# Kernel optimization log

Measured on AMD Instinct MI355X. Metric: run time of the kernel, lower is better.

The kernel has to match this reference:

```python
import jax, jax.numpy as jnp
import numpy as np

STRIDE = 2
IN_CH = 64
F_SCALE = 2
EMBED = 64  # int(in_ch * ss_exp_factor)


def _pixel_unshuffle(x, f):
    # out[b, (fi*f+fj)*c + cc, h, w] = x[b, cc, h*f+fi, w*f+fj]
    b, c, H, W = x.shape
    x = x.reshape(b, c, H // f, f, W // f, f)
    x = x.transpose(0, 3, 5, 1, 2, 4)  # b, fi, fj, c, h, w
    return x.reshape(b, f * f * c, H // f, W // f)


def _pixel_shuffle(x, f):
    b, fc, h, w = x.shape
    c = fc // (f * f)
    x = x.reshape(b, f, f, c, h, w)
    x = x.transpose(0, 3, 4, 1, 5, 2)  # b, c, h, fi, w, fj
    return x.reshape(b, c, h * f, w * f)


def _conv(x, w, b, dilation):
    out = jax.lax.conv_general_dilated(
        x, w, window_strides=(1, 1),
        padding=[(dilation, dilation), (dilation, dilation)],
        rhs_dilation=(dilation, dilation),
        dimension_numbers=('NCHW', 'OIHW', 'NCHW'))
    return out + b[None, :, None, None]


def _conv1x1(x, w, b):
    out = jax.lax.conv_general_dilated(
        x, w, window_strides=(1, 1), padding=[(0, 0), (0, 0)],
        dimension_numbers=('NCHW', 'OIHW', 'NCHW'))
    return out + b[None, :, None, None]


def _attention(x, wqk, f):
    b, c, H, W = x.shape
    # layer_norm over (c,h,w), no affine
    mu = jnp.mean(x, axis=(1, 2, 3), keepdims=True)
    var = jnp.var(x, axis=(1, 2, 3), keepdims=True)
    xx = (x - mu) / jnp.sqrt(var + 1e-5)
    ph, pw = (f - H % f) % f, (f - W % f) % f
    if ph or pw:
        xx = jnp.pad(xx, ((0, 0), (0, 0), (0, ph), (0, pw)))
        xv = jnp.pad(x, ((0, 0), (0, 0), (0, ph), (0, pw)))
    else:
        xv = x
    sh, sw = (H + ph) // f, (W + pw) // f
    B = b * f * f
    xu = _pixel_unshuffle(xx, f).reshape(B, c, sh, sw)
    vu = _pixel_unshuffle(xv, f).reshape(B, c, sh, sw)
    n = sh * sw
    qk = xu.transpose(0, 2, 3, 1).reshape(B, n, c)  # (B, n, c)
    v = vu.transpose(0, 2, 3, 1).reshape(B, n, c)
    q = qk @ wqk  # (B, n, e)
    q = q / jnp.maximum(jnp.linalg.norm(q, axis=-1, keepdims=True), 1e-12)
    attn = jnp.einsum('bne,bme->bnm', q, q) / jnp.sqrt(jnp.float32(wqk.shape[1]))
    attn = jax.nn.softmax(attn, axis=-1)
    out = jnp.einsum('bnm,bmc->bnc', attn, v)  # (B, n, c)
    out = out.reshape(B, sh, sw, c).transpose(0, 3, 1, 2)
    out = out.reshape(b, f * f * c, sh, sw)
    out = _pixel_shuffle(out, f)
    return out[:, :, :H, :W]


def setup_inputs() -> dict:
    key = jax.random.key(0)
    ks = jax.random.split(key, 8)
    c = IN_CH
    s3 = 1.0 / np.sqrt(c * 9)
    s1 = 1.0 / np.sqrt(c)
    return {
        'x': jax.random.normal(ks[0], (8, c, 128, 128), dtype=jnp.float32),
        'wqk': jax.random.normal(ks[1], (c, EMBED), dtype=jnp.float32) * np.sqrt(6.0 / (c + EMBED)),
        'conv1_w': jax.random.normal(ks[2], (c, c, 3, 3), dtype=jnp.float32) * s3,
        'conv1_b': jnp.zeros((c,), dtype=jnp.float32),
        'conv2_w': jax.random.normal(ks[3], (c, c, 3, 3), dtype=jnp.float32) * s3,
        'conv2_b': jnp.zeros((c,), dtype=jnp.float32),
        'conv3_w': jax.random.normal(ks[4], (c, c, 1, 1), dtype=jnp.float32) * s1,
        'conv3_b': jnp.zeros((c,), dtype=jnp.float32),
    }


def reference(x, wqk, conv1_w, conv1_b, conv2_w, conv2_b, conv3_w, conv3_b):
    f = F_SCALE * STRIDE
    a = x + _attention(x, wqk, f)
    y = jax.nn.relu(_conv(a, conv1_w, conv1_b, STRIDE))
    y = jax.nn.relu(_conv(y, conv2_w, conv2_b, STRIDE))
    y = _conv1x1(y, conv3_w, conv3_b)
    return x + y
```

## Files before the change

kernel.cpp:

```cpp
#include <hip/hip_runtime.h>

typedef unsigned short u16;
typedef unsigned int   u32;

typedef __attribute__((ext_vector_type(8))) short s16x8;
typedef __attribute__((ext_vector_type(4))) float f32x4;

__device__ __forceinline__ float bf2f(u16 u){
  union { u32 i; float f; } v; v.i = ((u32)u) << 16; return v.f;
}
__device__ __forceinline__ u16 f2bf(float f){
  union { float f; u32 i; } v; v.f = f;
  u32 x = v.i;
  return (u16)((x + 0x7fffu + ((x >> 16) & 1u)) >> 16);
}


__global__ __launch_bounds__(256) void k_lnstats(const float* __restrict__ x, float* __restrict__ stats){
  const int bb    = blockIdx.x >> 7;
  const int chunk = blockIdx.x & 127;
  const float4* p = (const float4*)(x + bb*1048576 + chunk*8192);
  float s = 0.f, ss = 0.f;
  #pragma unroll
  for (int i=0;i<8;++i){
    float4 v = p[threadIdx.x + (i<<8)];
    s  += v.x + v.y + v.z + v.w;
    ss += v.x*v.x + v.y*v.y + v.z*v.z + v.w*v.w;
  }
  #pragma unroll
  for (int off=32; off; off>>=1){ s += __shfl_down(s, off); ss += __shfl_down(ss, off); }
  __shared__ float rs[4], rss[4];
  const int lane = threadIdx.x & 63, wv = threadIdx.x >> 6;
  if (lane == 0){ rs[wv] = s; rss[wv] = ss; }
  __syncthreads();
  if (threadIdx.x == 0){
    atomicAdd(&stats[bb*2+0], rs[0]+rs[1]+rs[2]+rs[3]);
    atomicAdd(&stats[bb*2+1], rss[0]+rss[1]+rss[2]+rss[3]);
  }
}

__global__ __launch_bounds__(256) void k_wt(const float* __restrict__ w, u16* __restrict__ wt){
  int e = blockIdx.x*256 + threadIdx.x;
  int tap = e >> 12, co = (e >> 6) & 63, ci = e & 63;
  wt[e] = f2bf(w[(co*64 + ci)*9 + tap]);
}

__global__ __launch_bounds__(256) void k_qv(const float* __restrict__ x, const float* __restrict__ wqk,
                                            const float* __restrict__ stats,
                                            u16* __restrict__ qb, u16* __restrict__ vb){
  const int Bb = blockIdx.x >> 4;
  const int mt = blockIdx.x & 15;
  const int b = Bb >> 4, fi = (Bb >> 2) & 3, fj = Bb & 3;
  const float inv_n = 1.f/1048576.f;
  const float mu   = stats[2*b] * inv_n;
  const float var  = stats[2*b+1]*inv_n - mu*mu;
  const float rstd = rsqrtf(var + 1e-5f);

  __shared__ float xt[64][68];
  __shared__ float wk[64][68];
  __shared__ float red[64][17];
  const int t = threadIdx.x;
  const int m0 = mt << 6;

  #pragma unroll
  for (int i=0;i<16;++i){ int e = t+(i<<8); wk[e>>6][e&63] = wqk[e]; }
  #pragma unroll
  for (int i=0;i<16;++i){
    int e = t+(i<<8); int cc = e>>6, ml = e&63;
    int m = m0 + ml;
    int hh = ((m>>5)<<2)+fi, ww = ((m&31)<<2)+fj;
    xt[ml][cc] = (x[(((b<<6)+cc)<<14)+(hh<<7)+ww] - mu)*rstd;
  }
  __syncthreads();

  const int ty = t>>4, tx = t&15;
  float acc[4][4] = {};
  for (int cc=0; cc<64; ++cc){
    float a0=xt[(ty<<2)+0][cc], a1=xt[(ty<<2)+1][cc], a2=xt[(ty<<2)+2][cc], a3=xt[(ty<<2)+3][cc];
    float b0=wk[cc][(tx<<2)+0], b1=wk[cc][(tx<<2)+1], b2=wk[cc][(tx<<2)+2], b3=wk[cc][(tx<<2)+3];
    acc[0][0]+=a0*b0; acc[0][1]+=a0*b1; acc[0][2]+=a0*b2; acc[0][3]+=a0*b3;
    acc[1][0]+=a1*b0; acc[1][1]+=a1*b1; acc[1][2]+=a1*b2; acc[1][3]+=a1*b3;
    acc[2][0]+=a2*b0; acc[2][1]+=a2*b1; acc[2][2]+=a2*b2; acc[2][3]+=a2*b3;
    acc[3][0]+=a3*b0; acc[3][1]+=a3*b1; acc[3][2]+=a3*b2; acc[3][3]+=a3*b3;
  }
  #pragma unroll
  for (int i=0;i<4;++i){
    float pn = acc[i][0]*acc[i][0]+acc[i][1]*acc[i][1]+acc[i][2]*acc[i][2]+acc[i][3]*acc[i][3];
    red[(ty<<2)+i][tx] = pn;
  }
  __syncthreads();
  float inv[4];
  #pragma unroll
  for (int i=0;i<4;++i){
    float s = 0.f;
    #pragma unroll
    for (int k=0;k<16;++k) s += red[(ty<<2)+i][k];
    inv[i] = 1.f / fmaxf(sqrtf(s), 1e-12f);
  }
  #pragma unroll
  for (int i=0;i<4;++i)
    #pragma unroll
    for (int j=0;j<4;++j)
      xt[(ty<<2)+i][(tx<<2)+j] = acc[i][j]*inv[i];
  __syncthreads();
  #pragma unroll
  for (int i=0;i<16;++i){
    int e = t+(i<<8); int ml = e>>6, ee = e&63;
    qb[((Bb<<10)+m0+ml)*64 + ee] = f2bf(xt[ml][ee]);
  }
  #pragma unroll
  for (int i=0;i<16;++i){
    int e = t+(i<<8); int cc = e>>6, ml = e&63;
    int m = m0 + ml;
    int hh = ((m>>5)<<2)+fi, ww = ((m&31)<<2)+fj;
    wk[ml][cc] = x[(((b<<6)+cc)<<14)+(hh<<7)+ww];
  }
  __syncthreads();
  #pragma unroll
  for (int i=0;i<16;++i){
    int e = t+(i<<8); int cc = e>>6, ml = e&63;
    vb[(Bb<<16) + (cc<<10) + m0 + ml] = f2bf(wk[ml][cc]);
  }
}

__global__ __launch_bounds__(256) void k_attn(const u16* __restrict__ qb, const u16* __restrict__ vb,
                                              const float* __restrict__ x, u16* __restrict__ apad){
  const int bid = blockIdx.x;
  const int b   = bid & 7;
  const int rem = bid >> 3;
  const int qtp = rem >> 4;
  const int sub = rem & 15;
  const int Bb  = (b<<4) + sub;
  const int fi = (sub>>2)&3, fj = sub&3;
  const int qt0 = qtp << 1;
  __shared__ __align__(16) char lds[24576];
  const int KS = 0, VS = 8192, PS = 16384;

  const int t = threadIdx.x;
  const int w = t >> 6, lane = t & 63;
  const int lrow = lane & 15, lk = lane >> 4;

  const u16* qB = qb + (Bb<<16);
  const u16* vB = vb + (Bb<<16);

  s16x8 qf[2][2];
  #pragma unroll
  for (int t2=0; t2<2; ++t2){
    const u16* qrp = qB + (((qt0+t2)<<6) + (w<<4) + lrow)*64;
    qf[t2][0] = *(const s16x8*)(qrp + (lk<<3));
    qf[t2][1] = *(const s16x8*)(qrp + 32 + (lk<<3));
  }

  f32x4 o_acc[2][4] = {};
  float lp[2][4] = {};

  for (int kt=0; kt<16; ++kt){
    __syncthreads();
    #pragma unroll
    for (int c = t; c < 512; c += 256){
      int row = c >> 3, slot = c & 7;
      uint4 kv = *(const uint4*)(qB + ((kt<<6)+row)*64 + (slot<<3));
      *(uint4*)(lds + KS + row*128 + (((slot ^ (row&7)))<<4)) = kv;
      uint4 vv = *(const uint4*)(vB + (row<<10) + (kt<<6) + (slot<<3));
      *(uint4*)(lds + VS + row*128 + (((slot ^ (row&7)))<<4)) = vv;
    }
    __syncthreads();

    #pragma unroll
    for (int t2=0; t2<2; ++t2){
      f32x4 s_acc[4] = {};
      #pragma unroll
      for (int nt=0; nt<4; ++nt){
        int key = (nt<<4) + lrow;
        const char* kb = lds + KS + key*128;
        s16x8 kf0 = *(const s16x8*)(kb + ((lk       ^ (key&7))<<4));
        s16x8 kf1 = *(const s16x8*)(kb + (((4+lk)   ^ (key&7))<<4));
        s_acc[nt] = __builtin_amdgcn_mfma_f32_16x16x32_bf16(qf[t2][0], kf0, s_acc[nt], 0,0,0);
        s_acc[nt] = __builtin_amdgcn_mfma_f32_16x16x32_bf16(qf[t2][1], kf1, s_acc[nt], 0,0,0);
      }
      #pragma unroll
      for (int nt=0; nt<4; ++nt)
        #pragma unroll
        for (int r=0; r<4; ++r){
          float p = __expf(s_acc[nt][r]*0.125f);
          lp[t2][r] += p;
          int prow = (w<<4) + (lk<<2) + r;
          int key  = (nt<<4) + lrow;
          *(u16*)(lds + PS + prow*128 + ((key<<1) ^ ((prow&7)<<4))) = f2bf(p);
        }
      {
        int prow = (w<<4) + lrow;
        const char* pb = lds + PS + prow*128;
        s16x8 pf0 = *(const s16x8*)(pb + ((lk     ^ (prow&7))<<4));
        s16x8 pf1 = *(const s16x8*)(pb + (((4+lk) ^ (prow&7))<<4));
        #pragma unroll
        for (int nt=0; nt<4; ++nt){
          int ch = (nt<<4) + lrow;
          const char* vbp = lds + VS + ch*128;
          s16x8 vf0 = *(const s16x8*)(vbp + ((lk     ^ (ch&7))<<4));
          s16x8 vf1 = *(const s16x8*)(vbp + (((4+lk) ^ (ch&7))<<4));
          o_acc[t2][nt] = __builtin_amdgcn_mfma_f32_16x16x32_bf16(pf0, vf0, o_acc[t2][nt], 0,0,0);
          o_acc[t2][nt] = __builtin_amdgcn_mfma_f32_16x16x32_bf16(pf1, vf1, o_acc[t2][nt], 0,0,0);
        }
      }
    }
  }

  #pragma unroll
  for (int t2=0; t2<2; ++t2)
    #pragma unroll
    for (int r=0;r<4;++r){
      float s = lp[t2][r];
      s += __shfl_xor(s, 1); s += __shfl_xor(s, 2);
      s += __shfl_xor(s, 4); s += __shfl_xor(s, 8);
      lp[t2][r] = 1.f / s;
    }

  float* os = (float*)lds;
  #pragma unroll
  for (int t2=0; t2<2; ++t2){
    __syncthreads();
    #pragma unroll
    for (int nt=0; nt<4; ++nt)
      #pragma unroll
      for (int r=0; r<4; ++r)
        os[((w<<4)+(lk<<2)+r)*68 + (nt<<4)+lrow] = o_acc[t2][nt][r]*lp[t2][r];
    __syncthreads();
    const int m0 = (qt0+t2) << 6;
    #pragma unroll
    for (int i=0;i<16;++i){
      int e = t+(i<<8);
      int cc = e>>6, ml = e&63;
      int m = m0 + ml;
      int hh = ((m>>5)<<2)+fi, ww = ((m&31)<<2)+fj;
      os[ml*68 + cc] += x[(((b<<6)+cc)<<14) + (hh<<7) + ww];
    }
    __syncthreads();
    #pragma unroll
    for (int i=0;i<16;++i){
      int e = t+(i<<8);
      int ml = e>>6, cc = e&63;
      int m = m0 + ml;
      int hh = ((m>>5)<<2)+fi, ww = ((m&31)<<2)+fj;
      apad[((b*132 + hh+2)*132 + ww+2)*64 + cc] = f2bf(os[ml*68 + cc]);
    }
  }
}

__global__ __launch_bounds__(256) void k_conv3m(const u16* __restrict__ in, const u16* __restrict__ wt,
                                                const float* __restrict__ bias, u16* __restrict__ outp){
  const int bid = blockIdx.x;
  const int b   = bid & 7;
  const int r   = bid >> 3;
  const int h   = r & 127;
  const int seg = r >> 7;
  const int t = threadIdx.x;
  const int wv = t >> 6, lane = t & 63;
  const int lrow = lane & 15, lk = lane >> 4;
  const int co0 = wv << 4;
  const int w0 = seg << 6;

  s16x8 A[9][2];
  #pragma unroll
  for (int tap=0; tap<9; ++tap)
    #pragma unroll
    for (int hf=0; hf<2; ++hf)
      A[tap][hf] = *(const s16x8*)(wt + (((tap<<6) + co0 + lrow)<<6) + (hf<<5) + (lk<<3));

  float4 b4 = *(const float4*)&bias[co0 + (lk<<2)];
  f32x4 binit = {b4.x, b4.y, b4.z, b4.w};
  f32x4 acc[4] = {binit, binit, binit, binit};

  const int base_b = b * (132*132);
  #pragma unroll
  for (int dh=0; dh<3; ++dh){
    const u16* rowp = in + ((base_b + (h + (dh<<1))*132)<<6);
    #pragma unroll
    for (int dw=0; dw<3; ++dw){
      #pragma unroll
      for (int hf=0; hf<2; ++hf){
        #pragma unroll
        for (int pt=0; pt<4; ++pt){
          int wp = w0 + (pt<<4) + lrow + (dw<<1);
          s16x8 B = *(const s16x8*)(rowp + (wp<<6) + (hf<<5) + (lk<<3));
          acc[pt] = __builtin_amdgcn_mfma_f32_16x16x32_bf16(A[dh*3+dw][hf], B, acc[pt], 0,0,0);
        }
      }
    }
  }

  #pragma unroll
  for (int pt=0; pt<4; ++pt){
    int wp = w0 + (pt<<4) + lrow + 2;
    u16* op = outp + ((base_b + (h+2)*132 + wp)<<6) + co0 + (lk<<2);
    ushort4 o4;
    o4.x = f2bf(fmaxf(acc[pt][0], 0.f));
    o4.y = f2bf(fmaxf(acc[pt][1], 0.f));
    o4.z = f2bf(fmaxf(acc[pt][2], 0.f));
    o4.w = f2bf(fmaxf(acc[pt][3], 0.f));
    *(ushort4*)op = o4;
  }
}

__global__ __launch_bounds__(256) void k_conv1x1(const u16* __restrict__ y2, const float* __restrict__ w3,
                                                 const float* __restrict__ b3, const float* __restrict__ x,
                                                 float* __restrict__ out){
  const int b  = blockIdx.x >> 6;
  const int p0 = (blockIdx.x & 63) << 8;
  __shared__ u16  ys[256][68];
  __shared__ float w3s[64][68];
  __shared__ float bs[64];
  const int t = threadIdx.x;
  #pragma unroll
  for (int i=0;i<16;++i){ int e = t+(i<<8); w3s[e & 63][e >> 6] = w3[e]; }
  if (t < 64) bs[t] = b3[t];
  #pragma unroll
  for (int i=0;i<64;++i){
    int e = t + (i<<8);
    int px = e >> 6, ci = e & 63;
    int pg = p0 + px; int hh = pg >> 7, ww = pg & 127;
    ys[px][ci] = y2[((b*132 + hh+2)*132 + ww+2)*64 + ci];
  }
  __syncthreads();
  const int cog = (t >> 6) << 4;
  const int pl  = t & 63;
  float acc[16][4];
  #pragma unroll
  for (int c=0;c<16;++c){
    float bvv = bs[cog+c];
    acc[c][0]=bvv; acc[c][1]=bvv; acc[c][2]=bvv; acc[c][3]=bvv;
  }
  for (int c4=0;c4<64;c4+=4){
    float yv[4][4];
    #pragma unroll
    for (int p=0;p<4;++p){
      ushort4 u = *(const ushort4*)&ys[pl + (p<<6)][c4];
      yv[p][0]=bf2f(u.x); yv[p][1]=bf2f(u.y); yv[p][2]=bf2f(u.z); yv[p][3]=bf2f(u.w);
    }
    #pragma unroll
    for (int cq=0;cq<4;++cq){
      float4 w0 = *(const float4*)&w3s[c4+0][cog+(cq<<2)];
      float4 w1 = *(const float4*)&w3s[c4+1][cog+(cq<<2)];
      float4 w2 = *(const float4*)&w3s[c4+2][cog+(cq<<2)];
      float4 w3v = *(const float4*)&w3s[c4+3][cog+(cq<<2)];
      #pragma unroll
      for (int p=0;p<4;++p){
        acc[(cq<<2)+0][p] += yv[p][0]*w0.x + yv[p][1]*w1.x + yv[p][2]*w2.x + yv[p][3]*w3v.x;
        acc[(cq<<2)+1][p] += yv[p][0]*w0.y + yv[p][1]*w1.y + yv[p][2]*w2.y + yv[p][3]*w3v.y;
        acc[(cq<<2)+2][p] += yv[p][0]*w0.z + yv[p][1]*w1.z + yv[p][2]*w2.z + yv[p][3]*w3v.z;
        acc[(cq<<2)+3][p] += yv[p][0]*w0.w + yv[p][1]*w1.w + yv[p][2]*w2.w + yv[p][3]*w3v.w;
      }
    }
  }
  #pragma unroll
  for (int c=0;c<16;++c){
    int base = (((b<<6)+cog+c)<<14) + p0 + pl;
    #pragma unroll
    for (int p=0;p<4;++p){
      int gi = base + (p<<6);
      out[gi] = acc[c][p] + x[gi];
    }
  }
}

extern "C" void kernel_launch(void* const* d_in, const int* in_sizes, int n_in,
                              void* d_out, int out_size, void* d_ws, size_t ws_size,
                              hipStream_t stream){
  const float* x   = (const float*)d_in[0];
  const float* wqk = (const float*)d_in[1];
  const float* w1  = (const float*)d_in[2];
  const float* b1  = (const float*)d_in[3];
  const float* w2  = (const float*)d_in[4];
  const float* b2  = (const float*)d_in[5];
  const float* w3  = (const float*)d_in[6];
  const float* b3  = (const float*)d_in[7];
  float* out = (float*)d_out;

  float* stats = (float*)d_ws;
  u16* qb   = (u16*)((char*)d_ws + 256);
  u16* vb   = qb + 8388608;
  u16* apad = vb + 8388608;
  u16* y1   = qb;
  u16* y2   = apad;
  u16* wt1  = apad + 8921088;
  u16* wt2  = wt1 + 36864;

  hipMemsetAsync(stats, 0, 64, stream);
  k_wt<<<144, 256, 0, stream>>>(w1, wt1);
  k_wt<<<144, 256, 0, stream>>>(w2, wt2);
  k_lnstats<<<1024, 256, 0, stream>>>(x, stats);
  k_qv     <<<2048, 256, 0, stream>>>(x, wqk, stats, qb, vb);
  hipMemsetAsync(apad, 0, 17842176, stream);
  k_attn   <<<1024, 256, 0, stream>>>(qb, vb, x, apad);
  hipMemsetAsync(y1, 0, 17842176, stream);
  k_conv3m <<<2048, 256, 0, stream>>>(apad, wt1, b1, y1);
  k_conv3m <<<2048, 256, 0, stream>>>(y1, wt2, b2, y2);
  k_conv1x1<<<512, 256, 0, stream>>>(y2, w3, b3, x, out);
}
```

Baseline: 442.7 us.

## Keep attention probabilities in registers via transposed MFMA and permuted V layout

The attention kernel now computes S^T = K·Q^T so each lane's exp results already sit in the operand layout the P·V MFMA expects. It packs them with v_cvt_pk_bf16_f32 and feeds them directly, removing the LDS round-trip for P. The V buffer is written by k_qv in a permuted key order so the register-resident P matches V's k-dimension. Blocks grow to 512 threads, each wave handling one query tile, and the epilogue LDS stride changes to 69. This cuts LDS traffic and syncs per key tile, at the cost of fewer query tiles reusing each K/V load per wave.

```diff
diff --git a/kernel.cpp b/kernel.cpp
--- a/kernel.cpp
+++ b/kernel.cpp
@@ -5,6 +5,7 @@
 
 typedef __attribute__((ext_vector_type(8))) short s16x8;
 typedef __attribute__((ext_vector_type(4))) float f32x4;
+typedef __attribute__((ext_vector_type(4))) u32   u32x4;
 
 __device__ __forceinline__ float bf2f(u16 u){
   union { u32 i; float f; } v; v.i = ((u32)u) << 16; return v.f;
@@ -14,6 +15,7 @@
   u32 x = v.i;
   return (u16)((x + 0x7fffu + ((x >> 16) & 1u)) >> 16);
 }
+__device__ __forceinline__ s16x8 as_s16x8(u32x4 v){ return __builtin_bit_cast(s16x8, v); }
 
 
 __global__ __launch_bounds__(256) void k_lnstats(const float* __restrict__ x, float* __restrict__ stats){
@@ -119,11 +121,13 @@
   #pragma unroll
   for (int i=0;i<16;++i){
     int e = t+(i<<8); int cc = e>>6, ml = e&63;
-    vb[(Bb<<16) + (cc<<10) + m0 + ml] = f2bf(wk[ml][cc]);
-  }
-}
-
-__global__ __launch_bounds__(256) void k_attn(const u16* __restrict__ qb, const u16* __restrict__ vb,
+    int nt = ml>>4, ss = (ml>>2)&3, r = ml&3;
+    int sig = ((ss + ((nt>>1)<<2))<<3) + ((nt&1)<<2) + r;
+    vb[(Bb<<16) + (cc<<10) + m0 + sig] = f2bf(wk[ml][cc]);
+  }
+}
+
+__global__ __launch_bounds__(512) void k_attn(const u16* __restrict__ qb, const u16* __restrict__ vb,
                                               const float* __restrict__ x, u16* __restrict__ apad){
   const int bid = blockIdx.x;
   const int b   = bid & 7;
@@ -132,9 +136,8 @@
   const int sub = rem & 15;
   const int Bb  = (b<<4) + sub;
   const int fi = (sub>>2)&3, fj = sub&3;
-  const int qt0 = qtp << 1;
-  __shared__ __align__(16) char lds[24576];
-  const int KS = 0, VS = 8192, PS = 16384;
+  __shared__ __align__(16) char lds[17664];
+  const int KS = 0, VS = 8192;
 
   const int t = threadIdx.x;
   const int w = t >> 6, lane = t & 63;
@@ -143,106 +146,94 @@
   const u16* qB = qb + (Bb<<16);
   const u16* vB = vb + (Bb<<16);
 
-  s16x8 qf[2][2];
-  #pragma unroll
-  for (int t2=0; t2<2; ++t2){
-    const u16* qrp = qB + (((qt0+t2)<<6) + (w<<4) + lrow)*64;
-    qf[t2][0] = *(const s16x8*)(qrp + (lk<<3));
-    qf[t2][1] = *(const s16x8*)(qrp + 32 + (lk<<3));
-  }
-
-  f32x4 o_acc[2][4] = {};
-  float lp[2][4] = {};
+  const u16* qrp = qB + ((qtp<<7) + (w<<4) + lrow)*64;
+  const s16x8 qf0 = *(const s16x8*)(qrp + (lk<<3));
+  const s16x8 qf1 = *(const s16x8*)(qrp + 32 + (lk<<3));
+
+  f32x4 o_acc[4] = {};
+  float lp = 0.f;
 
   for (int kt=0; kt<16; ++kt){
     __syncthreads();
-    #pragma unroll
-    for (int c = t; c < 512; c += 256){
-      int row = c >> 3, slot = c & 7;
+    {
+      int row = t >> 3, slot = t & 7;
       uint4 kv = *(const uint4*)(qB + ((kt<<6)+row)*64 + (slot<<3));
-      *(uint4*)(lds + KS + row*128 + (((slot ^ (row&7)))<<4)) = kv;
+      *(uint4*)(lds + KS + row*128 + ((slot ^ (row&7))<<4)) = kv;
       uint4 vv = *(const uint4*)(vB + (row<<10) + (kt<<6) + (slot<<3));
-      *(uint4*)(lds + VS + row*128 + (((slot ^ (row&7)))<<4)) = vv;
-    }
-    __syncthreads();
-
-    #pragma unroll
-    for (int t2=0; t2<2; ++t2){
-      f32x4 s_acc[4] = {};
+      *(uint4*)(lds + VS + row*128 + ((slot ^ (row&7))<<4)) = vv;
+    }
+    __syncthreads();
+
+    u32x4 pa, pb;
+    #pragma unroll
+    for (int nt=0; nt<4; ++nt){
+      int key = (nt<<4) + lrow;
+      const char* kb = lds + KS + key*128;
+      s16x8 kf0 = *(const s16x8*)(kb + ((lk     ^ (key&7))<<4));
+      s16x8 kf1 = *(const s16x8*)(kb + (((4+lk) ^ (key&7))<<4));
+      f32x4 sa = {};
+      sa = __builtin_amdgcn_mfma_f32_16x16x32_bf16(kf0, qf0, sa, 0,0,0);
+      sa = __builtin_amdgcn_mfma_f32_16x16x32_bf16(kf1, qf1, sa, 0,0,0);
+      float p0 = __expf(sa[0]*0.125f), p1 = __expf(sa[1]*0.125f);
+      float p2 = __expf(sa[2]*0.125f), p3 = __expf(sa[3]*0.125f);
+      lp += (p0+p1)+(p2+p3);
+      u32 lo, hi;
+      asm("v_cvt_pk_bf16_f32 %0, %1, %2" : "=v"(lo) : "v"(p0), "v"(p1));
+      asm("v_cvt_pk_bf16_f32 %0, %1, %2" : "=v"(hi) : "v"(p2), "v"(p3));
+      if (nt==0){ pa[0]=lo; pa[1]=hi; }
+      else if (nt==1){ pa[2]=lo; pa[3]=hi; }
+      else if (nt==2){ pb[0]=lo; pb[1]=hi; }
+      else          { pb[2]=lo; pb[3]=hi; }
+    }
+    s16x8 pf0 = as_s16x8(pa), pf1 = as_s16x8(pb);
+
+    #pragma unroll
+    for (int nt=0; nt<4; ++nt){
+      int ch = (nt<<4) + lrow;
+      const char* vbp = lds + VS + ch*128;
+      s16x8 vf0 = *(const s16x8*)(vbp + ((lk     ^ (ch&7))<<4));
+      s16x8 vf1 = *(const s16x8*)(vbp + (((4+lk) ^ (ch&7))<<4));
+      o_acc[nt] = __builtin_amdgcn_mfma_f32_16x16x32_bf16(vf0, pf0, o_acc[nt], 0,0,0);
+      o_acc[nt] = __builtin_amdgcn_mfma_f32_16x16x32_bf16(vf1, pf1, o_acc[nt], 0,0,0);
+    }
+  }
+
+  {
+    float s = lp;
+    s += __shfl_xor(s, 16); s += __shfl_xor(s, 32);
+    lp = 1.f / s;
+  }
+
+  float* os = (float*)lds;
+  #pragma unroll
+  for (int half=0; half<2; ++half){
+    __syncthreads();
+    if ((w>>2) == half){
+      int ql = ((w&3)<<4) + lrow;
       #pragma unroll
-      for (int nt=0; nt<4; ++nt){
-        int key = (nt<<4) + lrow;
-        const char* kb = lds + KS + key*128;
-        s16x8 kf0 = *(const s16x8*)(kb + ((lk       ^ (key&7))<<4));
-        s16x8 kf1 = *(const s16x8*)(kb + (((4+lk)   ^ (key&7))<<4));
-        s_acc[nt] = __builtin_amdgcn_mfma_f32_16x16x32_bf16(qf[t2][0], kf0, s_acc[nt], 0,0,0);
-        s_acc[nt] = __builtin_amdgcn_mfma_f32_16x16x32_bf16(qf[t2][1], kf1, s_acc[nt], 0,0,0);
-      }
-      #pragma unroll
-      for (int nt=0; nt<4; ++nt)
+      for (int nt=0;nt<4;++nt)
         #pragma unroll
-        for (int r=0; r<4; ++r){
-          float p = __expf(s_acc[nt][r]*0.125f);
-          lp[t2][r] += p;
-          int prow = (w<<4) + (lk<<2) + r;
-          int key  = (nt<<4) + lrow;
-          *(u16*)(lds + PS + prow*128 + ((key<<1) ^ ((prow&7)<<4))) = f2bf(p);
-        }
-      {
-        int prow = (w<<4) + lrow;
-        const char* pb = lds + PS + prow*128;
-        s16x8 pf0 = *(const s16x8*)(pb + ((lk     ^ (prow&7))<<4));
-        s16x8 pf1 = *(const s16x8*)(pb + (((4+lk) ^ (prow&7))<<4));
-        #pragma unroll
-        for (int nt=0; nt<4; ++nt){
-          int ch = (nt<<4) + lrow;
-          const char* vbp = lds + VS + ch*128;
-          s16x8 vf0 = *(const s16x8*)(vbp + ((lk     ^ (ch&7))<<4));
-          s16x8 vf1 = *(const s16x8*)(vbp + (((4+lk) ^ (ch&7))<<4));
-          o_acc[t2][nt] = __builtin_amdgcn_mfma_f32_16x16x32_bf16(pf0, vf0, o_acc[t2][nt], 0,0,0);
-          o_acc[t2][nt] = __builtin_amdgcn_mfma_f32_16x16x32_bf16(pf1, vf1, o_acc[t2][nt], 0,0,0);
-        }
-      }
-    }
-  }
-
-  #pragma unroll
-  for (int t2=0; t2<2; ++t2)
-    #pragma unroll
-    for (int r=0;r<4;++r){
-      float s = lp[t2][r];
-      s += __shfl_xor(s, 1); s += __shfl_xor(s, 2);
-      s += __shfl_xor(s, 4); s += __shfl_xor(s, 8);
-      lp[t2][r] = 1.f / s;
-    }
-
-  float* os = (float*)lds;
-  #pragma unroll
-  for (int t2=0; t2<2; ++t2){
-    __syncthreads();
-    #pragma unroll
-    for (int nt=0; nt<4; ++nt)
-      #pragma unroll
-      for (int r=0; r<4; ++r)
-        os[((w<<4)+(lk<<2)+r)*68 + (nt<<4)+lrow] = o_acc[t2][nt][r]*lp[t2][r];
-    __syncthreads();
-    const int m0 = (qt0+t2) << 6;
-    #pragma unroll
-    for (int i=0;i<16;++i){
-      int e = t+(i<<8);
+        for (int r=0;r<4;++r)
+          os[ql*69 + (nt<<4)+(lk<<2)+r] = o_acc[nt][r]*lp;
+    }
+    __syncthreads();
+    const int m0 = (qtp<<7) + (half<<6);
+    #pragma unroll
+    for (int i=0;i<8;++i){
+      int e = t + (i<<9);
       int cc = e>>6, ml = e&63;
       int m = m0 + ml;
       int hh = ((m>>5)<<2)+fi, ww = ((m&31)<<2)+fj;
-      os[ml*68 + cc] += x[(((b<<6)+cc)<<14) + (hh<<7) + ww];
-    }
-    __syncthreads();
-    #pragma unroll
-    for (int i=0;i<16;++i){
-      int e = t+(i<<8);
+      os[ml*69 + cc] += x[(((b<<6)+cc)<<14) + (hh<<7) + ww];
+    }
+    __syncthreads();
+    #pragma unroll
+    for (int i=0;i<8;++i){
+      int e = t + (i<<9);
       int ml = e>>6, cc = e&63;
       int m = m0 + ml;
       int hh = ((m>>5)<<2)+fi, ww = ((m&31)<<2)+fj;
-      apad[((b*132 + hh+2)*132 + ww+2)*64 + cc] = f2bf(os[ml*68 + cc]);
+      apad[((b*132 + hh+2)*132 + ww+2)*64 + cc] = f2bf(os[ml*69 + cc]);
     }
   }
 }
@@ -391,7 +382,7 @@
   k_lnstats<<<1024, 256, 0, stream>>>(x, stats);
   k_qv     <<<2048, 256, 0, stream>>>(x, wqk, stats, qb, vb);
   hipMemsetAsync(apad, 0, 17842176, stream);
-  k_attn   <<<1024, 256, 0, stream>>>(qb, vb, x, apad);
+  k_attn   <<<1024, 512, 0, stream>>>(qb, vb, x, apad);
   hipMemsetAsync(y1, 0, 17842176, stream);
   k_conv3m <<<2048, 256, 0, stream>>>(apad, wt1, b1, y1);
   k_conv3m <<<2048, 256, 0, stream>>>(y1, wt2, b2, y2);
```

Measured after the change: 394.6 us. 10.9% less time.
